# Kernel tuning notes

Hardware: AMD Instinct MI355X
Metric: run time of the kernel (lower is better)

Reference implementation:

```python
import jax, jax.numpy as jnp
import numpy as np

HIDDEN = 2048
N_HEADS = 16
HEAD_DIM = 128
N_EXPERTS = 8
TOP_K = 2
INTER = 1024
EPS = 1e-5
ROPE_THETA = 10000.0
T = 2048


def rms_norm(x, w, eps=EPS):
    xf = x.astype(jnp.float32)
    return (xf * jax.lax.rsqrt(jnp.mean(xf * xf, axis=-1, keepdims=True) + eps)).astype(x.dtype) * w


def apply_rope(x, positions):
    # x: [T, H, D], NeoX-style half rotation
    d = x.shape[-1]
    inv_freq = 1.0 / (ROPE_THETA ** (jnp.arange(0, d, 2, dtype=jnp.float32) / d))
    ang = positions.astype(jnp.float32)[:, None] * inv_freq  # [T, D/2]
    cos = jnp.cos(ang)[:, None, :]
    sin = jnp.sin(ang)[:, None, :]
    x1, x2 = jnp.split(x, 2, axis=-1)
    return jnp.concatenate([x1 * cos - x2 * sin, x2 * cos + x1 * sin], axis=-1)


def setup_inputs() -> dict:
    key = jax.random.key(0)
    ks = jax.random.split(key, 8)
    s = 0.02
    return {
        "positions": jnp.arange(T, dtype=jnp.int32),
        "hidden_states": jax.random.normal(ks[0], (T, HIDDEN), jnp.float32),
        "qkv_w": jax.random.normal(ks[1], (3 * HIDDEN, HIDDEN), jnp.float32) * s,
        "o_w": jax.random.normal(ks[2], (HIDDEN, HIDDEN), jnp.float32) * s,
        "q_norm_w": jnp.ones((N_HEADS * HEAD_DIM,), jnp.float32),
        "k_norm_w": jnp.ones((N_HEADS * HEAD_DIM,), jnp.float32),
        "post_attn_norm_w": jnp.ones((HIDDEN,), jnp.float32),
        "post_ffn_norm_w": jnp.ones((HIDDEN,), jnp.float32),
        "gate_w": jax.random.normal(ks[3], (N_EXPERTS, HIDDEN), jnp.float32) * s,
        "w_gate": jax.random.normal(ks[4], (N_EXPERTS, INTER, HIDDEN), jnp.float32) * s,
        "w_up": jax.random.normal(ks[5], (N_EXPERTS, INTER, HIDDEN), jnp.float32) * s,
        "w_down": jax.random.normal(ks[6], (N_EXPERTS, HIDDEN, INTER), jnp.float32) * s,
    }


def attention(positions, x, qkv_w, o_w, q_norm_w, k_norm_w):
    qkv = x @ qkv_w.T  # [T, 3*HIDDEN]
    q, k, v = jnp.split(qkv, 3, axis=-1)
    q = rms_norm(q, q_norm_w)  # norm over full flat q dim (FlexOlmo/OLMoE style)
    k = rms_norm(k, k_norm_w)
    q = apply_rope(q.reshape(T, N_HEADS, HEAD_DIM), positions)
    k = apply_rope(k.reshape(T, N_HEADS, HEAD_DIM), positions)
    v = v.reshape(T, N_HEADS, HEAD_DIM)
    scale = 1.0 / np.sqrt(HEAD_DIM)
    scores = jnp.einsum('thd,shd->hts', q, k) * scale
    mask = jnp.tril(jnp.ones((T, T), bool))
    scores = jnp.where(mask[None], scores, -jnp.inf)
    p = jax.nn.softmax(scores, axis=-1)
    out = jnp.einsum('hts,shd->thd', p, v).reshape(T, HIDDEN)
    return out @ o_w.T


def moe(x, gate_w, w_gate, w_up, w_down):
    logits = (x @ gate_w.T).astype(jnp.float32)  # router_logits.float()
    probs = jax.nn.softmax(logits, axis=-1)
    topv, topi = jax.lax.top_k(probs, TOP_K)  # renormalize=False -> use raw softmax weights
    # dense per-expert combine weights: [T, E]
    wdense = jnp.zeros((T, N_EXPERTS), jnp.float32)
    wdense = jnp.sum(jax.nn.one_hot(topi, N_EXPERTS, dtype=jnp.float32) * topv[..., None], axis=1)
    # detach().clone() before dispatch (inference semantics: value unchanged)
    xe = jax.lax.stop_gradient(x)
    g = jnp.einsum('td,efd->tef', xe, w_gate)
    u = jnp.einsum('td,efd->tef', xe, w_up)
    h = jax.nn.silu(g) * u
    y = jnp.einsum('tef,edf->ted', h, w_down)
    return jnp.einsum('ted,te->td', y, wdense)


def reference(positions, hidden_states, qkv_w, o_w, q_norm_w, k_norm_w,
              post_attn_norm_w, post_ffn_norm_w, gate_w, w_gate, w_up, w_down):
    residual = hidden_states
    h = attention(positions, hidden_states, qkv_w, o_w, q_norm_w, k_norm_w)
    h = rms_norm(h, post_attn_norm_w)
    h = h + residual
    residual = h
    h = moe(h, gate_w, w_gate, w_up, w_down)
    h = rms_norm(h, post_ffn_norm_w)
    return residual + h
```

## Files before the change

kernel.cpp:

```cpp
#include <hip/hip_runtime.h>
#include <hip/hip_bf16.h>
#include <cmath>

#define TT 2048
#define HID 2048
#define NHEADS 16
#define HDIM 128
#define NEXP 8
#define INTERD 1024
#define EPSV 1e-5f

typedef short bf16x8 __attribute__((ext_vector_type(8)));
typedef float f32x4 __attribute__((ext_vector_type(4)));

__device__ __forceinline__ unsigned short f2bf(float f) {
    unsigned int u = __builtin_bit_cast(unsigned int, f);
    unsigned int r = (u + 0x7FFFu + ((u >> 16) & 1u)) >> 16;
    return (unsigned short)r;
}
__device__ __forceinline__ float bf2f(unsigned short h) {
    return __builtin_bit_cast(float, (unsigned int)h << 16);
}

__device__ __forceinline__ void gll16(const void* g, void* l) {
    __builtin_amdgcn_global_load_lds((const __attribute__((address_space(1))) void*)g,
                                     (__attribute__((address_space(3))) void*)l, 16, 0, 0);
}

__device__ __forceinline__ float block_reduce_sum_256(float v, float* red) {
    const int tid = threadIdx.x;
    red[tid] = v;
    __syncthreads();
    for (int s = 128; s > 0; s >>= 1) {
        if (tid < s) red[tid] += red[tid + s];
        __syncthreads();
    }
    float r = red[0];
    __syncthreads();
    return r;
}

__global__ __launch_bounds__(256) void split_f32k(const float* __restrict__ x,
                                                  unsigned short* __restrict__ hi,
                                                  unsigned short* __restrict__ lo, int n4) {
    int i = blockIdx.x * 256 + threadIdx.x;
    if (i >= n4) return;
    float4 v = reinterpret_cast<const float4*>(x)[i];
    float xs[4] = {v.x, v.y, v.z, v.w};
    unsigned short hs[4], ls[4];
#pragma unroll
    for (int u = 0; u < 4; ++u) {
        hs[u] = f2bf(xs[u]);
        ls[u] = f2bf(xs[u] - bf2f(hs[u]));
    }
    uint2 hp; hp.x = hs[0] | ((unsigned)hs[1] << 16); hp.y = hs[2] | ((unsigned)hs[3] << 16);
    uint2 lp; lp.x = ls[0] | ((unsigned)ls[1] << 16); lp.y = ls[2] | ((unsigned)ls[3] << 16);
    *reinterpret_cast<uint2*>(hi + (size_t)i * 4) = hp;
    *reinterpret_cast<uint2*>(lo + (size_t)i * 4) = lp;
}

#define BKS 32
__global__ __launch_bounds__(256) void gemm_sp(const unsigned short* __restrict__ Ah,
                                               const unsigned short* __restrict__ Al,
                                               const unsigned short* __restrict__ Bh,
                                               const unsigned short* __restrict__ Bl,
                                               float* __restrict__ C, int N, int K, int lda) {
    const int nbx = gridDim.x;
    const int nwg = nbx * gridDim.y;
    const int orig = blockIdx.y * nbx + blockIdx.x;
    const int qq = nwg >> 3, rr = nwg & 7;
    const int xcd = orig & 7, loc = orig >> 3;
    const int wgid = (xcd < rr ? xcd * (qq + 1) : rr * (qq + 1) + (xcd - rr) * qq) + loc;
    const int m0 = (wgid / nbx) * 128, n0 = (wgid % nbx) * 128;

    __shared__ __align__(16) unsigned short sAh[128 * BKS];
    __shared__ __align__(16) unsigned short sAl[128 * BKS];
    __shared__ __align__(16) unsigned short sBh[128 * BKS];
    __shared__ __align__(16) unsigned short sBl[128 * BKS];
    const int tid = threadIdx.x;
    const int w = tid >> 6, l = tid & 63;
    const int lr = l & 15, lg = l >> 4;
    const int wm = w >> 1, wn = w & 1;
    const int c0 = tid, c1 = tid + 256;
    const int r0 = c0 >> 2, s0 = (c0 & 3) * 8;
    const int r1 = c1 >> 2, s1 = (c1 & 3) * 8;
    const size_t a0 = (size_t)(m0 + r0) * lda + s0;
    const size_t a1 = (size_t)(m0 + r1) * lda + s1;
    const size_t b0 = (size_t)(n0 + r0) * K + s0;
    const size_t b1 = (size_t)(n0 + r1) * K + s1;

    f32x4 acc[4][4];
#pragma unroll
    for (int i = 0; i < 4; ++i)
#pragma unroll
        for (int j = 0; j < 4; ++j) acc[i][j] = f32x4{0.f, 0.f, 0.f, 0.f};

    for (int k0 = 0; k0 < K; k0 += BKS) {
        gll16(Ah + a0 + k0, &sAh[c0 * 8]);
        gll16(Ah + a1 + k0, &sAh[c1 * 8]);
        gll16(Al + a0 + k0, &sAl[c0 * 8]);
        gll16(Al + a1 + k0, &sAl[c1 * 8]);
        gll16(Bh + b0 + k0, &sBh[c0 * 8]);
        gll16(Bh + b1 + k0, &sBh[c1 * 8]);
        gll16(Bl + b0 + k0, &sBl[c0 * 8]);
        gll16(Bl + b1 + k0, &sBl[c1 * 8]);
        __syncthreads();
        bf16x8 bhf[4], blf[4];
#pragma unroll
        for (int nt = 0; nt < 4; ++nt) {
            int row = wn * 64 + nt * 16 + lr;
            bhf[nt] = *reinterpret_cast<const bf16x8*>(&sBh[row * BKS + lg * 8]);
            blf[nt] = *reinterpret_cast<const bf16x8*>(&sBl[row * BKS + lg * 8]);
        }
#pragma unroll
        for (int mt = 0; mt < 4; ++mt) {
            int row = wm * 64 + mt * 16 + lr;
            bf16x8 ahf = *reinterpret_cast<const bf16x8*>(&sAh[row * BKS + lg * 8]);
            bf16x8 alf = *reinterpret_cast<const bf16x8*>(&sAl[row * BKS + lg * 8]);
#pragma unroll
            for (int nt = 0; nt < 4; ++nt) {
                acc[mt][nt] = __builtin_amdgcn_mfma_f32_16x16x32_bf16(ahf, bhf[nt], acc[mt][nt], 0, 0, 0);
                acc[mt][nt] = __builtin_amdgcn_mfma_f32_16x16x32_bf16(ahf, blf[nt], acc[mt][nt], 0, 0, 0);
                acc[mt][nt] = __builtin_amdgcn_mfma_f32_16x16x32_bf16(alf, bhf[nt], acc[mt][nt], 0, 0, 0);
            }
        }
        __syncthreads();
    }
#pragma unroll
    for (int mt = 0; mt < 4; ++mt) {
#pragma unroll
        for (int r = 0; r < 4; ++r) {
            size_t crow = (size_t)(m0 + wm * 64 + mt * 16 + lg * 4 + r) * N;
#pragma unroll
            for (int nt = 0; nt < 4; ++nt)
                C[crow + n0 + wn * 64 + nt * 16 + lr] = acc[mt][nt][r];
        }
    }
}

__global__ __launch_bounds__(256) void gemm_moe(const float* __restrict__ A,
                                                const float* __restrict__ B,
                                                float* __restrict__ C,
                                                int N, int K, int lda,
                                                size_t strideB,
                                                const int* __restrict__ gather,
                                                const int* __restrict__ offs,
                                                const int* __restrict__ counts) {
    const int e = blockIdx.z;
    const int cnt = counts[e];
    const int base = offs[e];
    const int m0 = blockIdx.y * 128;
    if (m0 >= cnt) return;
    const int n0 = blockIdx.x * 128;
    const float* Bp = B + (size_t)e * strideB;

    __shared__ unsigned short smA[128 * 64];
    __shared__ unsigned short smB[128 * 64];
    __shared__ int rowsA[128];
    const int tid = threadIdx.x;
    if (tid < 128) {
        int rr = min(m0 + tid, cnt - 1);
        rowsA[tid] = gather ? gather[base + rr] : (base + rr);
    }
    __syncthreads();

    const int w = tid >> 6, l = tid & 63;
    const int lr = l & 15, lg = l >> 4;
    const int wm = w >> 1, wn = w & 1;
    char* sA = (char*)smA;
    char* sB = (char*)smB;

    f32x4 acc[4][4];
#pragma unroll
    for (int i = 0; i < 4; ++i)
#pragma unroll
        for (int j = 0; j < 4; ++j) acc[i][j] = f32x4{0.f, 0.f, 0.f, 0.f};

    for (int k0 = 0; k0 < K; k0 += 64) {
#pragma unroll
        for (int i = 0; i < 8; ++i) {
            int slot = tid + i * 256;
            int r = slot >> 4, kq = slot & 15;
            float4 av = *reinterpret_cast<const float4*>(&A[(size_t)rowsA[r] * lda + k0 + kq * 4]);
            uint2 pk;
            pk.x = (unsigned)f2bf(av.x) | ((unsigned)f2bf(av.y) << 16);
            pk.y = (unsigned)f2bf(av.z) | ((unsigned)f2bf(av.w) << 16);
            *reinterpret_cast<uint2*>(sA + r * 128 + ((kq * 8) ^ ((r & 7) << 4))) = pk;
        }
#pragma unroll
        for (int i = 0; i < 8; ++i) {
            int slot = tid + i * 256;
            int r = slot >> 4, kq = slot & 15;
            float4 bv = *reinterpret_cast<const float4*>(&Bp[(size_t)(n0 + r) * K + k0 + kq * 4]);
            uint2 pk;
            pk.x = (unsigned)f2bf(bv.x) | ((unsigned)f2bf(bv.y) << 16);
            pk.y = (unsigned)f2bf(bv.z) | ((unsigned)f2bf(bv.w) << 16);
            *reinterpret_cast<uint2*>(sB + r * 128 + ((kq * 8) ^ ((r & 7) << 4))) = pk;
        }
        __syncthreads();
#pragma unroll
        for (int kk = 0; kk < 2; ++kk) {
            bf16x8 af[4], bfr[4];
#pragma unroll
            for (int mt = 0; mt < 4; ++mt) {
                int row = wm * 64 + mt * 16 + lr;
                af[mt] = *reinterpret_cast<const bf16x8*>(sA + row * 128 + ((kk * 64 + lg * 16) ^ ((row & 7) << 4)));
            }
#pragma unroll
            for (int nt = 0; nt < 4; ++nt) {
                int row = wn * 64 + nt * 16 + lr;
                bfr[nt] = *reinterpret_cast<const bf16x8*>(sB + row * 128 + ((kk * 64 + lg * 16) ^ ((row & 7) << 4)));
            }
#pragma unroll
            for (int mt = 0; mt < 4; ++mt)
#pragma unroll
                for (int nt = 0; nt < 4; ++nt)
                    acc[mt][nt] = __builtin_amdgcn_mfma_f32_16x16x32_bf16(af[mt], bfr[nt], acc[mt][nt], 0, 0, 0);
        }
        __syncthreads();
    }
#pragma unroll
    for (int mt = 0; mt < 4; ++mt) {
#pragma unroll
        for (int r = 0; r < 4; ++r) {
            int rowl = wm * 64 + mt * 16 + lg * 4 + r;
            if (m0 + rowl < cnt) {
                size_t crow = (size_t)(base + m0 + rowl) * N;
#pragma unroll
                for (int nt = 0; nt < 4; ++nt)
                    C[crow + n0 + wn * 64 + nt * 16 + lr] = acc[mt][nt][r];
            }
        }
    }
}

__global__ __launch_bounds__(256) void qknorm_rope_split(float* __restrict__ qkv,
                                                         const float* __restrict__ qw,
                                                         const float* __restrict__ kw,
                                                         const int* __restrict__ pos) {
    __shared__ float xbuf[2048];
    __shared__ float red[256];
    const int t = blockIdx.x, tid = threadIdx.x;
    unsigned short* row16 = (unsigned short*)(qkv + (size_t)t * 6144);
    const float pf = (float)pos[t];
    float vreg[8];
    const float* vsrc = qkv + (size_t)t * 6144 + 4096;
#pragma unroll
    for (int i = 0; i < 8; ++i) vreg[i] = vsrc[tid + i * 256];
    __syncthreads();
#pragma unroll
    for (int i = 0; i < 8; ++i) {
        int d = tid + i * 256;
        unsigned short hi = f2bf(vreg[i]);
        row16[8192 + d] = hi;
        row16[10240 + d] = f2bf(vreg[i] - bf2f(hi));
    }
    for (int part = 0; part < 2; ++part) {
        const float* x = qkv + (size_t)t * 6144 + part * 2048;
        const float* wn = part ? kw : qw;
        const int sbase = part ? 4096 : 0;
        const float outscale = part ? 1.0f : 0.08838834764831845f;
        float s = 0.f;
#pragma unroll
        for (int i = 0; i < 8; ++i) {
            int d = tid + i * 256;
            float v = x[d];
            xbuf[d] = v;
            s = fmaf(v, v, s);
        }
        float tot = block_reduce_sum_256(s, red);
        float scale = rsqrtf(tot * (1.f / HID) + EPSV);
#pragma unroll
        for (int p = tid; p < 1024; p += 256) {
            int hh = p >> 6, j = p & 63;
            int i1 = hh * 128 + j, i2 = i1 + 64;
            float x1 = xbuf[i1] * scale * wn[i1];
            float x2 = xbuf[i2] * scale * wn[i2];
            float invf = expf(-(float)j * 0.14391156831212787f);
            float ang = pf * invf;
            float sn, cs;
            sincosf(ang, &sn, &cs);
            float o1 = (x1 * cs - x2 * sn) * outscale;
            float o2 = (x2 * cs + x1 * sn) * outscale;
            unsigned short h1_ = f2bf(o1);
            row16[sbase + i1] = h1_;
            row16[sbase + 2048 + i1] = f2bf(o1 - bf2f(h1_));
            unsigned short h2_ = f2bf(o2);
            row16[sbase + i2] = h2_;
            row16[sbase + 2048 + i2] = f2bf(o2 - bf2f(h2_));
        }
        __syncthreads();
    }
}

__global__ __launch_bounds__(256) void kvprep(const unsigned short* __restrict__ qkv16,
                                              unsigned short* __restrict__ kt,
                                              unsigned short* __restrict__ vt) {
    const int C = blockIdx.x;
    const int h = blockIdx.y;
    const int tid = threadIdx.x;
#pragma unroll
    for (int p = 0; p < 2; ++p) {
#pragma unroll
        for (int i = 0; i < 4; ++i) {
            int slot = tid + i * 256;
            int r = slot >> 4, sg = slot & 15;
            uint4 v = *reinterpret_cast<const uint4*>(
                qkv16 + (size_t)(C * 64 + r) * 12288 + 4096 + p * 2048 + h * 128 + (sg ^ (r & 7)) * 8);
            *reinterpret_cast<uint4*>(kt + (size_t)(h * 32 + C) * 16384 + p * 8192 + slot * 8) = v;
        }
    }
    __shared__ unsigned short tile[64 * 128];
    char* tb = (char*)tile;
    for (int p = 0; p < 2; ++p) {
#pragma unroll
        for (int i = 0; i < 4; ++i) {
            int c = tid + i * 256;
            int r = c >> 4, dseg = c & 15;
            uint4 v = *reinterpret_cast<const uint4*>(
                qkv16 + (size_t)(C * 64 + r) * 12288 + 8192 + p * 2048 + h * 128 + dseg * 8);
            int swz = dseg ^ (r & 7) ^ (r >> 3);
            *reinterpret_cast<uint4*>(tb + r * 256 + swz * 16) = v;
        }
        __syncthreads();
        unsigned short* ob = vt + (size_t)(h * 32 + C) * 16384 + p * 8192;
#pragma unroll
        for (int i = 0; i < 4; ++i) {
            int c = tid + i * 256;
            int d = c >> 3, j = c & 7;
            unsigned short tmp[8];
#pragma unroll
            for (int u = 0; u < 8; ++u) {
                int s = 8 * j + u;
                int swz = (d >> 3) ^ (s & 7) ^ (s >> 3);
                tmp[u] = *reinterpret_cast<const unsigned short*>(tb + s * 256 + swz * 16 + (d & 7) * 2);
            }
            *reinterpret_cast<uint4*>(ob + (size_t)d * 64 + ((j ^ (d & 7)) * 8)) =
                *reinterpret_cast<const uint4*>(tmp);
        }
        __syncthreads();
    }
}

#define STAGE(BUF, CIDX)                                                          \
    {                                                                             \
        const unsigned short* kb_ = kt + (size_t)(h * 32 + (CIDX)) * 16384;       \
        const unsigned short* vb_ = vt + (size_t)(h * 32 + (CIDX)) * 16384;       \
        char* kd_ = kvb + (BUF) * 65536;                                          \
        char* vd_ = kd_ + 32768;                                                  \
        _Pragma("unroll")                                                         \
        for (int p_ = 0; p_ < 2; ++p_) {                                          \
            _Pragma("unroll")                                                     \
            for (int i_ = 0; i_ < 4; ++i_) {                                      \
                int slot_ = tid + i_ * 256;                                       \
                gll16(kb_ + p_ * 8192 + slot_ * 8, kd_ + p_ * 16384 + slot_ * 16);\
                gll16(vb_ + p_ * 8192 + slot_ * 8, vd_ + p_ * 16384 + slot_ * 16);\
            }                                                                     \
        }                                                                         \
    }

__global__ __launch_bounds__(256) void attn_mfma(const unsigned short* __restrict__ qkv16,
                                                 const unsigned short* __restrict__ kt,
                                                 const unsigned short* __restrict__ vt,
                                                 unsigned short* __restrict__ oh,
                                                 unsigned short* __restrict__ ol) {
    const int g = blockIdx.x;
    const int rank = (g < 256) ? g : 767 - g;
    const int h = rank & 15;
    const int t0 = (31 - (rank >> 4)) * 64;
    const int tid = threadIdx.x;
    const int w = tid >> 6, l = tid & 63;
    const int lr = l & 15, lg = l >> 4;
    const size_t RS = 12288;
    __shared__ __align__(16) unsigned short KVd[65536];
    __shared__ unsigned short Ps[4][2 * 16 * 64];
    char* kvb = (char*)KVd;
    char* PsB = (char*)(Ps[w]);

    bf16x8 qh[4], ql[4];
    {
        const unsigned short* qp = qkv16 + (size_t)(t0 + w * 16 + lr) * RS + h * 128 + lg * 8;
#pragma unroll
        for (int kk = 0; kk < 4; ++kk) {
            qh[kk] = *reinterpret_cast<const bf16x8*>(qp + kk * 32);
            ql[kk] = *reinterpret_cast<const bf16x8*>(qp + 2048 + kk * 32);
        }
    }
    f32x4 oacc[8];
#pragma unroll
    for (int dt = 0; dt < 8; ++dt) oacc[dt] = f32x4{0.f, 0.f, 0.f, 0.f};
    float mrun[4] = {-INFINITY, -INFINITY, -INFINITY, -INFINITY};
    float lrun[4] = {0.f, 0.f, 0.f, 0.f};

    STAGE(0, 0);
    int cur = 0;
    for (int s0 = 0; s0 <= t0; s0 += 64) {
        if (s0 + 64 <= t0) {
            STAGE(cur ^ 1, (s0 >> 6) + 1);
            asm volatile("s_waitcnt vmcnt(16)" ::: "memory");
        } else {
            asm volatile("s_waitcnt vmcnt(0)" ::: "memory");
        }
        __builtin_amdgcn_s_barrier();
        __builtin_amdgcn_sched_barrier(0);
        char* KsB = kvb + cur * 65536;
        char* VtB = KsB + 32768;

        f32x4 sc[4];
        __builtin_amdgcn_s_setprio(1);
#pragma unroll
        for (int nt = 0; nt < 4; ++nt) {
            f32x4 a = f32x4{0.f, 0.f, 0.f, 0.f};
#pragma unroll
            for (int kk = 0; kk < 4; ++kk) {
                int row = nt * 16 + lr;
                int off = row * 256 + ((kk * 64 + lg * 16) ^ ((row & 7) << 4));
                bf16x8 kh = *reinterpret_cast<const bf16x8*>(KsB + off);
                bf16x8 kl = *reinterpret_cast<const bf16x8*>(KsB + 16384 + off);
                a = __builtin_amdgcn_mfma_f32_16x16x32_bf16(qh[kk], kh, a, 0, 0, 0);
                a = __builtin_amdgcn_mfma_f32_16x16x32_bf16(qh[kk], kl, a, 0, 0, 0);
                a = __builtin_amdgcn_mfma_f32_16x16x32_bf16(ql[kk], kh, a, 0, 0, 0);
            }
            sc[nt] = a;
        }
        __builtin_amdgcn_s_setprio(0);
        float mnew[4], alpha[4], psum[4];
#pragma unroll
        for (int r = 0; r < 4; ++r) {
            int row_t = t0 + w * 16 + lg * 4 + r;
            float mx = mrun[r];
#pragma unroll
            for (int nt = 0; nt < 4; ++nt) {
                int col = s0 + nt * 16 + lr;
                float v = sc[nt][r];
                if (col > row_t) v = -INFINITY;
                sc[nt][r] = v;
                mx = fmaxf(mx, v);
            }
#pragma unroll
            for (int o = 1; o < 16; o <<= 1) mx = fmaxf(mx, __shfl_xor(mx, o));
            mnew[r] = mx;
            alpha[r] = expf(mrun[r] - mx);
            mrun[r] = mx;
            psum[r] = 0.f;
        }
#pragma unroll
        for (int nt = 0; nt < 4; ++nt) {
#pragma unroll
            for (int r = 0; r < 4; ++r) {
                float p = expf(sc[nt][r] - mnew[r]);
                psum[r] += p;
                int prow = lg * 4 + r;
                int off = prow * 128 + (((nt * 16 + lr) * 2) ^ ((prow & 7) << 4));
                unsigned short ph = f2bf(p);
                *reinterpret_cast<unsigned short*>(PsB + off) = ph;
                *reinterpret_cast<unsigned short*>(PsB + 2048 + off) = f2bf(p - bf2f(ph));
            }
        }
#pragma unroll
        for (int r = 0; r < 4; ++r) {
            float s = psum[r];
#pragma unroll
            for (int o = 1; o < 16; o <<= 1) s += __shfl_xor(s, o);
            lrun[r] = lrun[r] * alpha[r] + s;
        }
#pragma unroll
        for (int dt = 0; dt < 8; ++dt)
#pragma unroll
            for (int r = 0; r < 4; ++r) oacc[dt][r] *= alpha[r];
        bf16x8 ph[2], pl[2];
#pragma unroll
        for (int kk = 0; kk < 2; ++kk) {
            int off = lr * 128 + ((kk * 64 + lg * 16) ^ ((lr & 7) << 4));
            ph[kk] = *reinterpret_cast<const bf16x8*>(PsB + off);
            pl[kk] = *reinterpret_cast<const bf16x8*>(PsB + 2048 + off);
        }
        __builtin_amdgcn_s_setprio(1);
#pragma unroll
        for (int dt = 0; dt < 8; ++dt) {
            int row = dt * 16 + lr;
#pragma unroll
            for (int kk = 0; kk < 2; ++kk) {
                int off = row * 128 + ((kk * 64 + lg * 16) ^ ((row & 7) << 4));
                bf16x8 vh = *reinterpret_cast<const bf16x8*>(VtB + off);
                bf16x8 vl = *reinterpret_cast<const bf16x8*>(VtB + 16384 + off);
                oacc[dt] = __builtin_amdgcn_mfma_f32_16x16x32_bf16(ph[kk], vh, oacc[dt], 0, 0, 0);
                oacc[dt] = __builtin_amdgcn_mfma_f32_16x16x32_bf16(ph[kk], vl, oacc[dt], 0, 0, 0);
                oacc[dt] = __builtin_amdgcn_mfma_f32_16x16x32_bf16(pl[kk], vh, oacc[dt], 0, 0, 0);
            }
        }
        __builtin_amdgcn_s_setprio(0);
        asm volatile("s_waitcnt lgkmcnt(0)" ::: "memory");
        __builtin_amdgcn_s_barrier();
        __builtin_amdgcn_sched_barrier(0);
        cur ^= 1;
    }
#pragma unroll
    for (int r = 0; r < 4; ++r) {
        float inv = 1.f / lrun[r];
        int row_t = t0 + w * 16 + lg * 4 + r;
#pragma unroll
        for (int dt = 0; dt < 8; ++dt) {
            float o = oacc[dt][r] * inv;
            unsigned short hb = f2bf(o);
            size_t idx = (size_t)row_t * 2048 + h * 128 + dt * 16 + lr;
            oh[idx] = hb;
            ol[idx] = f2bf(o - bf2f(hb));
        }
    }
}

__global__ __launch_bounds__(256) void add_rmsnorm(const float* __restrict__ resid,
                                                   const float* __restrict__ x,
                                                   const float* __restrict__ w,
                                                   float* __restrict__ out) {
    __shared__ float red[256];
    const int t = blockIdx.x, tid = threadIdx.x;
    const float* xr = x + (size_t)t * HID;
    float v[8];
    float s = 0.f;
#pragma unroll
    for (int i = 0; i < 8; ++i) { v[i] = xr[tid + i * 256]; s = fmaf(v[i], v[i], s); }
    float tot = block_reduce_sum_256(s, red);
    float scale = rsqrtf(tot * (1.f / HID) + EPSV);
#pragma unroll
    for (int i = 0; i < 8; ++i) {
        int d = tid + i * 256;
        out[(size_t)t * HID + d] = resid[(size_t)t * HID + d] + v[i] * scale * w[d];
    }
}

__global__ __launch_bounds__(64) void router_kernel(const float* __restrict__ h1,
                                                    const float* __restrict__ gate_w,
                                                    int* __restrict__ topi, float* __restrict__ topv,
                                                    int* __restrict__ slot_tk, int* __restrict__ counts) {
    const int t = blockIdx.x, lane = threadIdx.x;
    float acc[NEXP] = {};
    const float* x = h1 + (size_t)t * HID;
    for (int d = lane; d < HID; d += 64) {
        float xv = x[d];
#pragma unroll
        for (int e = 0; e < NEXP; ++e) acc[e] = fmaf(xv, gate_w[e * HID + d], acc[e]);
    }
#pragma unroll
    for (int e = 0; e < NEXP; ++e)
#pragma unroll
        for (int off = 32; off > 0; off >>= 1) acc[e] += __shfl_down(acc[e], off);
    if (lane == 0) {
        float mx = acc[0];
        for (int e = 1; e < NEXP; ++e) mx = fmaxf(mx, acc[e]);
        float p[NEXP], se = 0.f;
        for (int e = 0; e < NEXP; ++e) { p[e] = expf(acc[e] - mx); se += p[e]; }
        float inv = 1.f / se;
        for (int e = 0; e < NEXP; ++e) p[e] *= inv;
        int e1 = 0;
        for (int e = 1; e < NEXP; ++e) if (p[e] > p[e1]) e1 = e;
        int e2 = (e1 == 0) ? 1 : 0;
        for (int e = 0; e < NEXP; ++e) if (e != e1 && p[e] > p[e2]) e2 = e;
        topi[t * 2] = e1;     topv[t * 2] = p[e1];
        topi[t * 2 + 1] = e2; topv[t * 2 + 1] = p[e2];
        slot_tk[t * 2]     = atomicAdd(&counts[e1], 1);
        slot_tk[t * 2 + 1] = atomicAdd(&counts[e2], 1);
    }
}

__global__ void scan_kernel(const int* __restrict__ counts, int* __restrict__ offs) {
    int o = 0;
    for (int e = 0; e < NEXP; ++e) { offs[e] = o; o += counts[e]; }
}

__global__ __launch_bounds__(256) void map_kernel(const int* __restrict__ topi,
                                                  const int* __restrict__ slot_tk,
                                                  const int* __restrict__ offs,
                                                  int* __restrict__ token_of_row,
                                                  int* __restrict__ row_of_tk) {
    int idx = blockIdx.x * 256 + threadIdx.x;
    if (idx >= TT * 2) return;
    int e = topi[idx];
    int row = offs[e] + slot_tk[idx];
    token_of_row[row] = idx >> 1;
    row_of_tk[idx] = row;
}

__global__ __launch_bounds__(256) void silu_mul(float* __restrict__ g, const float* __restrict__ u, int n4) {
    int i = blockIdx.x * 256 + threadIdx.x;
    if (i >= n4) return;
    float4 gv = reinterpret_cast<float4*>(g)[i];
    float4 uv = reinterpret_cast<const float4*>(u)[i];
    gv.x = gv.x / (1.f + expf(-gv.x)) * uv.x;
    gv.y = gv.y / (1.f + expf(-gv.y)) * uv.y;
    gv.z = gv.z / (1.f + expf(-gv.z)) * uv.z;
    gv.w = gv.w / (1.f + expf(-gv.w)) * uv.w;
    reinterpret_cast<float4*>(g)[i] = gv;
}

__global__ __launch_bounds__(256) void final_combine(const float* __restrict__ h1,
                                                     const float* __restrict__ ypart,
                                                     const float* __restrict__ topv,
                                                     const int* __restrict__ row_of_tk,
                                                     const float* __restrict__ wffn,
                                                     float* __restrict__ out) {
    __shared__ float red[256];
    const int t = blockIdx.x, tid = threadIdx.x;
    const int r0 = row_of_tk[t * 2], r1 = row_of_tk[t * 2 + 1];
    const float w0 = topv[t * 2], w1 = topv[t * 2 + 1];
    const float* y0 = ypart + (size_t)r0 * HID;
    const float* y1 = ypart + (size_t)r1 * HID;
    float v[8];
    float s = 0.f;
#pragma unroll
    for (int i = 0; i < 8; ++i) {
        int d = tid + i * 256;
        v[i] = w0 * y0[d] + w1 * y1[d];
        s = fmaf(v[i], v[i], s);
    }
    float tot = block_reduce_sum_256(s, red);
    float scale = rsqrtf(tot * (1.f / HID) + EPSV);
#pragma unroll
    for (int i = 0; i < 8; ++i) {
        int d = tid + i * 256;
        out[(size_t)t * HID + d] = h1[(size_t)t * HID + d] + v[i] * scale * wffn[d];
    }
}

extern "C" void kernel_launch(void* const* d_in, const int* in_sizes, int n_in,
                              void* d_out, int out_size, void* d_ws, size_t ws_size,
                              hipStream_t stream) {
    const int*   positions = (const int*)d_in[0];
    const float* hidden    = (const float*)d_in[1];
    const float* qkv_w     = (const float*)d_in[2];
    const float* o_w       = (const float*)d_in[3];
    const float* q_norm_w  = (const float*)d_in[4];
    const float* k_norm_w  = (const float*)d_in[5];
    const float* post_attn = (const float*)d_in[6];
    const float* post_ffn  = (const float*)d_in[7];
    const float* gate_w    = (const float*)d_in[8];
    const float* w_gate    = (const float*)d_in[9];
    const float* w_up      = (const float*)d_in[10];
    const float* w_down    = (const float*)d_in[11];
    float* out = (float*)d_out;

    char* ws = (char*)d_ws;
    size_t off = 0;
    auto alloc = [&](size_t bytes) -> void* {
        void* p = ws + off;
        off += (bytes + 255) & ~(size_t)255;
        return p;
    };
    float*          qkvbuf = (float*)alloc((size_t)TT * 6144 * 4);
    unsigned short* hidsp  = (unsigned short*)alloc((size_t)TT * HID * 2 * 2);
    unsigned short* wsp    = (unsigned short*)alloc(((size_t)6144 * HID * 2 + (size_t)HID * HID * 2) * 2);
    float*          h1     = (float*)alloc((size_t)TT * HID * 4);
    int*   topi   = (int*)alloc(TT * 2 * 4);
    float* topv   = (float*)alloc(TT * 2 * 4);
    int*   slot   = (int*)alloc(TT * 2 * 4);
    int*   rowtk  = (int*)alloc(TT * 2 * 4);
    int*   tokrow = (int*)alloc(TT * 2 * 4);
    int*   counts = (int*)alloc(8 * 4);
    int*   offsb  = (int*)alloc(8 * 4);
    if (off > ws_size) return;

    unsigned short* hid_hi   = hidsp;
    unsigned short* hid_lo   = hidsp + (size_t)TT * HID;
    unsigned short* attnO_hi = hid_hi;
    unsigned short* attnO_lo = hid_lo;
    unsigned short* qkvw_hi = wsp;
    unsigned short* qkvw_lo = wsp + (size_t)6144 * HID;
    unsigned short* ow_hi   = wsp + (size_t)2 * 6144 * HID;
    unsigned short* ow_lo   = ow_hi + (size_t)HID * HID;
    unsigned short* vtbuf   = wsp;
    unsigned short* ktbuf   = wsp + (size_t)TT * HID * 2;
    float* gbuf  = qkvbuf;
    float* ubuf  = qkvbuf + (size_t)4096 * INTERD;
    float* oOut  = qkvbuf + (size_t)8192 * INTERD;
    float* ypart = oOut;

    hipMemsetAsync(counts, 0, 8 * sizeof(int), stream);

    dim3 b256(256);
    split_f32k<<<dim3(TT * HID / 4 / 256), b256, 0, stream>>>(hidden, hid_hi, hid_lo, TT * HID / 4);
    split_f32k<<<dim3(6144 * HID / 4 / 256), b256, 0, stream>>>(qkv_w, qkvw_hi, qkvw_lo, 6144 * HID / 4);
    split_f32k<<<dim3(HID * HID / 4 / 256), b256, 0, stream>>>(o_w, ow_hi, ow_lo, HID * HID / 4);
    gemm_sp<<<dim3(6144 / 128, TT / 128), b256, 0, stream>>>(hid_hi, hid_lo, qkvw_hi, qkvw_lo,
                                                             qkvbuf, 6144, HID, HID);
    qknorm_rope_split<<<dim3(TT), b256, 0, stream>>>(qkvbuf, q_norm_w, k_norm_w, positions);
    kvprep<<<dim3(32, NHEADS), b256, 0, stream>>>((const unsigned short*)qkvbuf, ktbuf, vtbuf);
    attn_mfma<<<dim3(512), b256, 0, stream>>>((const unsigned short*)qkvbuf, ktbuf, vtbuf,
                                              attnO_hi, attnO_lo);
    gemm_sp<<<dim3(HID / 128, TT / 128), b256, 0, stream>>>(attnO_hi, attnO_lo, ow_hi, ow_lo,
                                                            oOut, HID, HID, HID);
    add_rmsnorm<<<dim3(TT), b256, 0, stream>>>(hidden, oOut, post_attn, h1);
    router_kernel<<<dim3(TT), dim3(64), 0, stream>>>(h1, gate_w, topi, topv, slot, counts);
    scan_kernel<<<1, 1, 0, stream>>>(counts, offsb);
    map_kernel<<<dim3((TT * 2 + 255) / 256), b256, 0, stream>>>(topi, slot, offsb, tokrow, rowtk);
    gemm_moe<<<dim3(INTERD / 128, 32, NEXP), b256, 0, stream>>>(
        h1, w_gate, gbuf, INTERD, HID, HID, (size_t)INTERD * HID, tokrow, offsb, counts);
    gemm_moe<<<dim3(INTERD / 128, 32, NEXP), b256, 0, stream>>>(
        h1, w_up, ubuf, INTERD, HID, HID, (size_t)INTERD * HID, tokrow, offsb, counts);
    silu_mul<<<dim3((TT * 2 * INTERD / 4 + 255) / 256), b256, 0, stream>>>(gbuf, ubuf, TT * 2 * INTERD / 4);
    gemm_moe<<<dim3(HID / 128, 32, NEXP), b256, 0, stream>>>(
        gbuf, w_down, ypart, HID, INTERD, INTERD, (size_t)HID * INTERD, nullptr, offsb, counts);
    final_combine<<<dim3(TT), b256, 0, stream>>>(h1, ypart, topv, rowtk, post_ffn, out);
}
```

Baseline: 781.4 us.

## Double GEMM K-tile with swizzled LDS and single-buffer attention KV staging

The split-precision GEMM now stages a 64-wide K tile with an XOR-swizzled LDS layout, which halves the number of loop iterations and barriers and is meant to reduce LDS bank conflicts. The attention kernel drops its double-buffered K/V prefetch in favour of a single buffer loaded synchronously each iteration. That halves the attention LDS footprint, which may allow more resident workgroups, and reorders the score MFMA loop to run nt innermost. The cost is that global-load latency is no longer overlapped with compute in attention, and GEMM LDS usage doubles.

Result: faster. 729.0 us (-6.7%).

```diff
diff --git a/kernel.cpp b/kernel.cpp
--- a/kernel.cpp
+++ b/kernel.cpp
@@ -59,7 +59,7 @@
     *reinterpret_cast<uint2*>(lo + (size_t)i * 4) = lp;
 }
 
-#define BKS 32
+#define BKS 64
 __global__ __launch_bounds__(256) void gemm_sp(const unsigned short* __restrict__ Ah,
                                                const unsigned short* __restrict__ Al,
                                                const unsigned short* __restrict__ Bh,
@@ -81,13 +81,6 @@
     const int w = tid >> 6, l = tid & 63;
     const int lr = l & 15, lg = l >> 4;
     const int wm = w >> 1, wn = w & 1;
-    const int c0 = tid, c1 = tid + 256;
-    const int r0 = c0 >> 2, s0 = (c0 & 3) * 8;
-    const int r1 = c1 >> 2, s1 = (c1 & 3) * 8;
-    const size_t a0 = (size_t)(m0 + r0) * lda + s0;
-    const size_t a1 = (size_t)(m0 + r1) * lda + s1;
-    const size_t b0 = (size_t)(n0 + r0) * K + s0;
-    const size_t b1 = (size_t)(n0 + r1) * K + s1;
 
     f32x4 acc[4][4];
 #pragma unroll
@@ -96,32 +89,39 @@
         for (int j = 0; j < 4; ++j) acc[i][j] = f32x4{0.f, 0.f, 0.f, 0.f};
 
     for (int k0 = 0; k0 < K; k0 += BKS) {
-        gll16(Ah + a0 + k0, &sAh[c0 * 8]);
-        gll16(Ah + a1 + k0, &sAh[c1 * 8]);
-        gll16(Al + a0 + k0, &sAl[c0 * 8]);
-        gll16(Al + a1 + k0, &sAl[c1 * 8]);
-        gll16(Bh + b0 + k0, &sBh[c0 * 8]);
-        gll16(Bh + b1 + k0, &sBh[c1 * 8]);
-        gll16(Bl + b0 + k0, &sBl[c0 * 8]);
-        gll16(Bl + b1 + k0, &sBl[c1 * 8]);
-        __syncthreads();
-        bf16x8 bhf[4], blf[4];
-#pragma unroll
-        for (int nt = 0; nt < 4; ++nt) {
-            int row = wn * 64 + nt * 16 + lr;
-            bhf[nt] = *reinterpret_cast<const bf16x8*>(&sBh[row * BKS + lg * 8]);
-            blf[nt] = *reinterpret_cast<const bf16x8*>(&sBl[row * BKS + lg * 8]);
-        }
-#pragma unroll
-        for (int mt = 0; mt < 4; ++mt) {
-            int row = wm * 64 + mt * 16 + lr;
-            bf16x8 ahf = *reinterpret_cast<const bf16x8*>(&sAh[row * BKS + lg * 8]);
-            bf16x8 alf = *reinterpret_cast<const bf16x8*>(&sAl[row * BKS + lg * 8]);
+#pragma unroll
+        for (int i = 0; i < 4; ++i) {
+            int c = tid + i * 256;
+            int r = c >> 3, z = c & 7;
+            int ko = k0 + (((z ^ (r & 7)) & 7) << 3);
+            gll16(Ah + (size_t)(m0 + r) * lda + ko, (char*)sAh + c * 16);
+            gll16(Al + (size_t)(m0 + r) * lda + ko, (char*)sAl + c * 16);
+            gll16(Bh + (size_t)(n0 + r) * K + ko,   (char*)sBh + c * 16);
+            gll16(Bl + (size_t)(n0 + r) * K + ko,   (char*)sBl + c * 16);
+        }
+        __syncthreads();
+#pragma unroll
+        for (int kk = 0; kk < 2; ++kk) {
+            bf16x8 bhf[4], blf[4];
 #pragma unroll
             for (int nt = 0; nt < 4; ++nt) {
-                acc[mt][nt] = __builtin_amdgcn_mfma_f32_16x16x32_bf16(ahf, bhf[nt], acc[mt][nt], 0, 0, 0);
-                acc[mt][nt] = __builtin_amdgcn_mfma_f32_16x16x32_bf16(ahf, blf[nt], acc[mt][nt], 0, 0, 0);
-                acc[mt][nt] = __builtin_amdgcn_mfma_f32_16x16x32_bf16(alf, bhf[nt], acc[mt][nt], 0, 0, 0);
+                int row = wn * 64 + nt * 16 + lr;
+                int off = row * 128 + ((kk * 64 + lg * 16) ^ ((row & 7) << 4));
+                bhf[nt] = *reinterpret_cast<const bf16x8*>((const char*)sBh + off);
+                blf[nt] = *reinterpret_cast<const bf16x8*>((const char*)sBl + off);
+            }
+#pragma unroll
+            for (int mt = 0; mt < 4; ++mt) {
+                int row = wm * 64 + mt * 16 + lr;
+                int off = row * 128 + ((kk * 64 + lg * 16) ^ ((row & 7) << 4));
+                bf16x8 ahf = *reinterpret_cast<const bf16x8*>((const char*)sAh + off);
+                bf16x8 alf = *reinterpret_cast<const bf16x8*>((const char*)sAl + off);
+#pragma unroll
+                for (int nt = 0; nt < 4; ++nt) {
+                    acc[mt][nt] = __builtin_amdgcn_mfma_f32_16x16x32_bf16(ahf, bhf[nt], acc[mt][nt], 0, 0, 0);
+                    acc[mt][nt] = __builtin_amdgcn_mfma_f32_16x16x32_bf16(ahf, blf[nt], acc[mt][nt], 0, 0, 0);
+                    acc[mt][nt] = __builtin_amdgcn_mfma_f32_16x16x32_bf16(alf, bhf[nt], acc[mt][nt], 0, 0, 0);
+                }
             }
         }
         __syncthreads();
@@ -342,21 +342,19 @@
     }
 }
 
-#define STAGE(BUF, CIDX)                                                          \
-    {                                                                             \
-        const unsigned short* kb_ = kt + (size_t)(h * 32 + (CIDX)) * 16384;       \
-        const unsigned short* vb_ = vt + (size_t)(h * 32 + (CIDX)) * 16384;       \
-        char* kd_ = kvb + (BUF) * 65536;                                          \
-        char* vd_ = kd_ + 32768;                                                  \
-        _Pragma("unroll")                                                         \
-        for (int p_ = 0; p_ < 2; ++p_) {                                          \
-            _Pragma("unroll")                                                     \
-            for (int i_ = 0; i_ < 4; ++i_) {                                      \
-                int slot_ = tid + i_ * 256;                                       \
-                gll16(kb_ + p_ * 8192 + slot_ * 8, kd_ + p_ * 16384 + slot_ * 16);\
-                gll16(vb_ + p_ * 8192 + slot_ * 8, vd_ + p_ * 16384 + slot_ * 16);\
-            }                                                                     \
-        }                                                                         \
+#define STAGE1(CIDX)                                                                   \
+    {                                                                                  \
+        const unsigned short* kb_ = kt + (size_t)(h * 32 + (CIDX)) * 16384;            \
+        const unsigned short* vb_ = vt + (size_t)(h * 32 + (CIDX)) * 16384;            \
+        _Pragma("unroll")                                                              \
+        for (int p_ = 0; p_ < 2; ++p_) {                                               \
+            _Pragma("unroll")                                                          \
+            for (int i_ = 0; i_ < 4; ++i_) {                                           \
+                int slot_ = tid + i_ * 256;                                            \
+                gll16(kb_ + p_ * 8192 + slot_ * 8, kvb + p_ * 16384 + slot_ * 16);     \
+                gll16(vb_ + p_ * 8192 + slot_ * 8, kvb + 32768 + p_ * 16384 + slot_ * 16); \
+            }                                                                          \
+        }                                                                              \
     }
 
 __global__ __launch_bounds__(256) void attn_mfma(const unsigned short* __restrict__ qkv16,
@@ -372,9 +370,9 @@
     const int w = tid >> 6, l = tid & 63;
     const int lr = l & 15, lg = l >> 4;
     const size_t RS = 12288;
-    __shared__ __align__(16) unsigned short KVd[65536];
+    __shared__ __align__(16) unsigned short KVs[32768];
     __shared__ unsigned short Ps[4][2 * 16 * 64];
-    char* kvb = (char*)KVd;
+    char* kvb = (char*)KVs;
     char* PsB = (char*)(Ps[w]);
 
     bf16x8 qh[4], ql[4];
@@ -392,36 +390,28 @@
     float mrun[4] = {-INFINITY, -INFINITY, -INFINITY, -INFINITY};
     float lrun[4] = {0.f, 0.f, 0.f, 0.f};
 
-    STAGE(0, 0);
-    int cur = 0;
     for (int s0 = 0; s0 <= t0; s0 += 64) {
-        if (s0 + 64 <= t0) {
-            STAGE(cur ^ 1, (s0 >> 6) + 1);
-            asm volatile("s_waitcnt vmcnt(16)" ::: "memory");
-        } else {
-            asm volatile("s_waitcnt vmcnt(0)" ::: "memory");
-        }
-        __builtin_amdgcn_s_barrier();
-        __builtin_amdgcn_sched_barrier(0);
-        char* KsB = kvb + cur * 65536;
-        char* VtB = KsB + 32768;
+        STAGE1(s0 >> 6);
+        __syncthreads();
+        char* KsB = kvb;
+        char* VtB = kvb + 32768;
 
         f32x4 sc[4];
+#pragma unroll
+        for (int nt = 0; nt < 4; ++nt) sc[nt] = f32x4{0.f, 0.f, 0.f, 0.f};
         __builtin_amdgcn_s_setprio(1);
 #pragma unroll
-        for (int nt = 0; nt < 4; ++nt) {
-            f32x4 a = f32x4{0.f, 0.f, 0.f, 0.f};
-#pragma unroll
-            for (int kk = 0; kk < 4; ++kk) {
+        for (int kk = 0; kk < 4; ++kk) {
+#pragma unroll
+            for (int nt = 0; nt < 4; ++nt) {
                 int row = nt * 16 + lr;
                 int off = row * 256 + ((kk * 64 + lg * 16) ^ ((row & 7) << 4));
                 bf16x8 kh = *reinterpret_cast<const bf16x8*>(KsB + off);
                 bf16x8 kl = *reinterpret_cast<const bf16x8*>(KsB + 16384 + off);
-                a = __builtin_amdgcn_mfma_f32_16x16x32_bf16(qh[kk], kh, a, 0, 0, 0);
-                a = __builtin_amdgcn_mfma_f32_16x16x32_bf16(qh[kk], kl, a, 0, 0, 0);
-                a = __builtin_amdgcn_mfma_f32_16x16x32_bf16(ql[kk], kh, a, 0, 0, 0);
-            }
-            sc[nt] = a;
+                sc[nt] = __builtin_amdgcn_mfma_f32_16x16x32_bf16(qh[kk], kh, sc[nt], 0, 0, 0);
+                sc[nt] = __builtin_amdgcn_mfma_f32_16x16x32_bf16(ql[kk], kh, sc[nt], 0, 0, 0);
+                sc[nt] = __builtin_amdgcn_mfma_f32_16x16x32_bf16(qh[kk], kl, sc[nt], 0, 0, 0);
+            }
         }
         __builtin_amdgcn_s_setprio(0);
         float mnew[4], alpha[4], psum[4];
@@ -490,10 +480,7 @@
             }
         }
         __builtin_amdgcn_s_setprio(0);
-        asm volatile("s_waitcnt lgkmcnt(0)" ::: "memory");
-        __builtin_amdgcn_s_barrier();
-        __builtin_amdgcn_sched_barrier(0);
-        cur ^= 1;
+        __syncthreads();
     }
 #pragma unroll
     for (int r = 0; r < 4; ++r) {
```
